# Kernel optimization log

Measured on AMD Instinct MI355X. Metric: run time of the kernel, lower is better.

Reference implementation:

```python
import jax, jax.numpy as jnp
import numpy as np

IN_F = 4096
OUT_F = 4096
RANK = 16
ALPHA = 32
BLOCK = 64  # quantization blocksize along in_features
SCALING = ALPHA / RANK


def setup_inputs() -> dict:
    key = jax.random.key(0)
    k1, k2, k3, k4, k5, k6 = jax.random.split(key, 6)
    x = jax.random.normal(k1, (4, 2048, IN_F), dtype=jnp.float32)
    # int4 codes stored with +8 offset, values in [0, 16)
    q_codes = jax.random.randint(k2, (OUT_F, IN_F), 0, 16, dtype=jnp.int32)
    # per-(row, block) dequant scales
    scales = jax.random.uniform(k3, (OUT_F, IN_F // BLOCK), dtype=jnp.float32) * 0.02
    bias = jax.random.normal(k4, (OUT_F,), dtype=jnp.float32) * 0.02
    lora_A = jax.random.normal(k5, (RANK, IN_F), dtype=jnp.float32) * (1.0 / np.sqrt(IN_F))
    lora_B = jax.random.normal(k6, (OUT_F, RANK), dtype=jnp.float32) * 0.02
    return {"x": x, "q_codes": q_codes, "scales": scales, "bias": bias,
            "lora_A": lora_A, "lora_B": lora_B}


def _dequant(q_codes, scales):
    # [O, I] int4 codes (offset by 8) -> fp32 weight via blockwise scales
    O, I = q_codes.shape
    c = (q_codes.astype(jnp.float32) - 8.0).reshape(O, I // BLOCK, BLOCK)
    return (c * scales[:, :, None]).reshape(O, I)


def reference(x, q_codes, scales, bias, lora_A, lora_B):
    w = _dequant(q_codes, scales)                      # [O, I]
    base = jnp.einsum('bsi,oi->bso', x, w) + bias      # dequant GEMM + bias
    # LoRA branch: dropout(p=0) is identity; x @ (B@A).T == (x @ A.T) @ B.T
    lora = jnp.einsum('bsr,or->bso', jnp.einsum('bsi,ri->bsr', x, lora_A), lora_B)
    return base + lora * SCALING
```

## Files before the change

### kernel.cpp

```cpp
#include <hip/hip_runtime.h>
#include <hip/hip_bf16.h>

#define IN_F   4096
#define OUT_F  4096
#define RANK   16
#define M_TOK  8192
#define SCALING 2.0f

typedef __attribute__((ext_vector_type(8)))  short short8;
typedef __attribute__((ext_vector_type(4)))  float f32x4;
typedef __attribute__((ext_vector_type(16))) float f32x16;
typedef __attribute__((ext_vector_type(4)))  float fvec4;
typedef __attribute__((ext_vector_type(4)))  int   ivec4;
typedef __attribute__((ext_vector_type(4)))  unsigned int uvec4;

__global__ __launch_bounds__(256) void cvt_x(const float* __restrict__ x,
                                             __hip_bfloat16* __restrict__ xb) {
    const size_t nvec = (size_t)M_TOK * IN_F / 8;
    const size_t stride = (size_t)gridDim.x * 256;
    for (size_t idx = (size_t)blockIdx.x * 256 + threadIdx.x; idx < nvec; idx += stride) {
        const size_t i = idx * 8;
        fvec4 a = __builtin_nontemporal_load((const fvec4*)(x + i));
        fvec4 b = __builtin_nontemporal_load((const fvec4*)(x + i + 4));
        union { uvec4 u; __hip_bfloat16 h[8]; } p;
        p.h[0] = __float2bfloat16(a.x);
        p.h[1] = __float2bfloat16(a.y);
        p.h[2] = __float2bfloat16(a.z);
        p.h[3] = __float2bfloat16(a.w);
        p.h[4] = __float2bfloat16(b.x);
        p.h[5] = __float2bfloat16(b.y);
        p.h[6] = __float2bfloat16(b.z);
        p.h[7] = __float2bfloat16(b.w);
        *(uvec4*)(xb + i) = p.u;
    }
}

__global__ __launch_bounds__(256) void dequant_lora(const int* __restrict__ q,
                                                    const float* __restrict__ sc,
                                                    const float* __restrict__ lA,
                                                    const float* __restrict__ lB,
                                                    __hip_bfloat16* __restrict__ W) {
    const int tid = threadIdx.x;
    const int id  = blockIdx.x;
    const int c0  = (id & 3) * 1024 + tid * 4;
    const int o0  = (id >> 2) * 8;

    ivec4 qv[8];
#pragma unroll
    for (int oo = 0; oo < 8; ++oo)
        qv[oo] = __builtin_nontemporal_load(
            (const ivec4*)(q + (size_t)(o0 + oo) * IN_F + c0));

    float sv[8];
#pragma unroll
    for (int oo = 0; oo < 8; ++oo)
        sv[oo] = sc[(o0 + oo) * (IN_F / 64) + (c0 >> 6)];

    fvec4 a[RANK];
#pragma unroll
    for (int r = 0; r < RANK; ++r)
        a[r] = *(const fvec4*)(lA + (size_t)r * IN_F + c0);

#pragma unroll
    for (int oo = 0; oo < 8; ++oo) {
        const float* lbo = lB + (size_t)(o0 + oo) * RANK;
        float l0 = 0.f, l1 = 0.f, l2 = 0.f, l3 = 0.f;
#pragma unroll
        for (int r = 0; r < RANK; ++r) {
            const float br = lbo[r];
            l0 += br * a[r].x; l1 += br * a[r].y;
            l2 += br * a[r].z; l3 += br * a[r].w;
        }
        const float s = sv[oo];
        union { ushort4 u; __hip_bfloat16 h[4]; } p;
        p.h[0] = __float2bfloat16((float)(qv[oo].x - 8) * s + SCALING * l0);
        p.h[1] = __float2bfloat16((float)(qv[oo].y - 8) * s + SCALING * l1);
        p.h[2] = __float2bfloat16((float)(qv[oo].z - 8) * s + SCALING * l2);
        p.h[3] = __float2bfloat16((float)(qv[oo].w - 8) * s + SCALING * l3);
        *(ushort4*)(W + (size_t)(o0 + oo) * IN_F + c0) = p.u;
    }
}


__device__ __forceinline__ void load_lds16(const void* g, void* l) {
    __builtin_amdgcn_global_load_lds(
        (const __attribute__((address_space(1))) unsigned int*)g,
        (__attribute__((address_space(3))) unsigned int*)l, 16, 0, 0);
}

#define MFMA32 __builtin_amdgcn_mfma_f32_32x32x16_bf16

__global__ __launch_bounds__(512, 2) void gemm256_8ph(const __hip_bfloat16* __restrict__ A,
                                                      const __hip_bfloat16* __restrict__ B,
                                                      const float* __restrict__ bias,
                                                      float* __restrict__ C) {
    extern __shared__ __align__(16) char lds[];

    const int tid  = threadIdx.x;
    const int lane = tid & 63;
    const int wave = tid >> 6;

    const int xcd = blockIdx.x & 7;
    const int w64 = blockIdx.x >> 3;
    const int tm  = (xcd >> 1) * 8 + (w64 >> 3);
    const int tn  = (xcd & 1) * 8 + (w64 & 7);

    const __hip_bfloat16* Ab = A + (size_t)tm * 256 * IN_F;
    const __hip_bfloat16* Bb = B + (size_t)tn * 256 * IN_F;

    const int srow = ((lane >> 2) & 15) + ((lane & 1) << 4) + ((wave >> 2) << 5);
    const int skc  = ((((lane >> 1) ^ (lane >> 5)) & 1) << 3) + ((wave & 3) << 4);
    const size_t off0 = (size_t)srow * IN_F + (size_t)skc;

    const __hip_bfloat16* qA0 = Ab + off0;
    const __hip_bfloat16* qA1 = Ab + (size_t)128 * IN_F + off0;
    const __hip_bfloat16* qB0 = Bb + off0;
    const __hip_bfloat16* qB1 = Bb + (size_t)128 * IN_F + off0;

    const int flo32 = (lane & 16)
                    + (((((lane >> 5) ^ (lane >> 3)) & 1)) << 5)
                    + ((lane & 15) << 6);

    const int ah = wave >> 2;
    const int bh = (wave >> 1) & 1;

    const char* aRd[2] = { lds + ah * 16384 + flo32,
                           lds + 65536 + ah * 16384 + flo32 };
    const char* bRd[2] = { lds + 32768 + bh * 16384 + (wave & 1) * 8192 + flo32,
                           lds + 65536 + 32768 + bh * 16384 + (wave & 1) * 8192 + flo32 };

    const int wv1024 = wave * 1024;

#define STAGE2(ps, te, LO) do {                                             \
        const __hip_bfloat16* g_ = (ps) + (te);                             \
        load_lds16(g_,              lds + (LO) + wv1024);                   \
        load_lds16(g_ + 64 * IN_F,  lds + (LO) + 8192 + wv1024);            \
    } while (0)

    STAGE2(qB0, 0,  32768);
    STAGE2(qB1, 0,  49152);
    STAGE2(qA0, 0,  0);
    STAGE2(qA1, 0,  16384);
    STAGE2(qB0, 64, 65536 + 32768);
    STAGE2(qB1, 64, 65536 + 49152);
    asm volatile("s_waitcnt vmcnt(4)" ::: "memory");
    __builtin_amdgcn_s_barrier();

    short8 aF[2][4], bA[4], bB[4];
    f32x16 acc[4][2] = {};

#define TILE(T, CBI) do {                                                          \
        const int t1e = (((T) + 1) & 63) << 6;        \
        const int t2e = (((T) + 2) & 63) << 6;                                     \
                          \
        _Pragma("unroll")                                                          \
        for (int i = 0; i < 2; ++i)                                                \
            _Pragma("unroll")                                                      \
            for (int ks = 0; ks < 4; ++ks)                                         \
                aF[i][ks] = *(const short8*)(aRd[CBI] + i * 4096 + ks * 1024);     \
        _Pragma("unroll")                                                          \
        for (int ks = 0; ks < 4; ++ks)                                             \
            bA[ks] = *(const short8*)(bRd[CBI] + ks * 1024);                       \
        STAGE2(qA0, t1e, ((CBI) ^ 1) * 65536);                                     \
        __builtin_amdgcn_s_setprio(1);                                             \
        _Pragma("unroll")                                                          \
        for (int ks = 0; ks < 4; ++ks) {                                           \
            acc[0][0] = MFMA32(aF[0][ks], bA[ks], acc[0][0], 0, 0, 0);             \
            acc[1][0] = MFMA32(aF[1][ks], bA[ks], acc[1][0], 0, 0, 0);             \
        }                                                                          \
        __builtin_amdgcn_s_setprio(0);                                             \
        __builtin_amdgcn_s_barrier();                     \
                          \
        _Pragma("unroll")                                                          \
        for (int ks = 0; ks < 4; ++ks)                                             \
            bB[ks] = *(const short8*)(bRd[CBI] + 4096 + ks * 1024);                \
        STAGE2(qA1, t1e, ((CBI) ^ 1) * 65536 + 16384);                             \
        __builtin_amdgcn_s_setprio(1);                                             \
        _Pragma("unroll")                                                          \
        for (int ks = 0; ks < 4; ++ks) {                                           \
            acc[0][1] = MFMA32(aF[0][ks], bB[ks], acc[0][1], 0, 0, 0);             \
            acc[1][1] = MFMA32(aF[1][ks], bB[ks], acc[1][1], 0, 0, 0);             \
        }                                                                          \
        __builtin_amdgcn_s_setprio(0);                                             \
        __builtin_amdgcn_s_barrier();                     \
                          \
        _Pragma("unroll")                                                          \
        for (int i = 0; i < 2; ++i)                                                \
            _Pragma("unroll")                                                      \
            for (int ks = 0; ks < 4; ++ks)                                         \
                aF[i][ks] = *(const short8*)(aRd[CBI] + 8192 + i * 4096 + ks * 1024);\
        STAGE2(qB0, t2e, (CBI) * 65536 + 32768);       \
        __builtin_amdgcn_s_setprio(1);                                             \
        _Pragma("unroll")                                                          \
        for (int ks = 0; ks < 4; ++ks) {                                           \
            acc[2][1] = MFMA32(aF[0][ks], bB[ks], acc[2][1], 0, 0, 0);             \
            acc[3][1] = MFMA32(aF[1][ks], bB[ks], acc[3][1], 0, 0, 0);             \
        }                                                                          \
        __builtin_amdgcn_s_setprio(0);                                             \
        __builtin_amdgcn_s_barrier();                \
                          \
        STAGE2(qB1, t2e, (CBI) * 65536 + 49152);       \
        asm volatile("s_waitcnt vmcnt(4)" ::: "memory");      \
        __builtin_amdgcn_s_barrier();                \
        __builtin_amdgcn_s_setprio(1);                                             \
        _Pragma("unroll")                                                          \
        for (int ks = 0; ks < 4; ++ks) {                                           \
            acc[2][0] = MFMA32(aF[0][ks], bA[ks], acc[2][0], 0, 0, 0);             \
            acc[3][0] = MFMA32(aF[1][ks], bA[ks], acc[3][0], 0, 0, 0);             \
        }                                                                          \
        __builtin_amdgcn_s_setprio(0);                                             \
                    \
    } while (0)

    for (int tt = 0; tt < 32; ++tt) {
        TILE(2 * tt,     0);
        TILE(2 * tt + 1, 1);
    }
    asm volatile("s_waitcnt vmcnt(0)" ::: "memory");

    const int cl = lane & 31;
    const int hi = lane >> 5;
    const size_t m_base = (size_t)tm * 256 + (size_t)ah * 128 + hi * 4;
    const int    n_base = tn * 256 + (wave & 3) * 64;
#pragma unroll
    for (int cb = 0; cb < 2; ++cb) {
        const int n = n_base + cb * 32 + cl;
        const float bv = bias[n];
#pragma unroll
        for (int rb = 0; rb < 4; ++rb) {
#pragma unroll
            for (int g = 0; g < 4; ++g) {
                const size_t m0 = m_base + rb * 32 + g * 8;
#pragma unroll
                for (int rr = 0; rr < 4; ++rr)
                    __builtin_nontemporal_store(acc[rb][cb][g * 4 + rr] + bv,
                                                &C[(m0 + rr) * OUT_F + n]);
            }
        }
    }
#undef STAGE2
#undef TILE
}

extern "C" void kernel_launch(void* const* d_in, const int* in_sizes, int n_in,
                              void* d_out, int out_size, void* d_ws, size_t ws_size,
                              hipStream_t stream) {
    const float* x    = (const float*)d_in[0];
    const int*   qc   = (const int*)d_in[1];
    const float* sc   = (const float*)d_in[2];
    const float* bias = (const float*)d_in[3];
    const float* lA   = (const float*)d_in[4];
    const float* lB   = (const float*)d_in[5];
    float* out = (float*)d_out;

    __hip_bfloat16* xb = (__hip_bfloat16*)d_ws;
    __hip_bfloat16* wb = xb + (size_t)M_TOK * IN_F;

    static bool attr_done = false;
    if (!attr_done) {
        (void)hipFuncSetAttribute((const void*)gemm256_8ph,
                                  hipFuncAttributeMaxDynamicSharedMemorySize, 131072);
        attr_done = true;
    }

    cvt_x<<<2048, 256, 0, stream>>>(x, xb);
    dequant_lora<<<2048, 256, 0, stream>>>(qc, sc, lA, lB, wb);
    gemm256_8ph<<<dim3(512), dim3(512), 131072, stream>>>(xb, wb, bias, out);
}
```

Measured before the change: 491.2 us.

## Triple-buffer B tiles in LDS and drop intra-tile barriers

The LDS layout changes from two A/B buffer pairs to two A buffers plus three B buffers, raising dynamic shared memory to 160 KB. The main loop is unrolled with a 6-tile rotation so B buffers cycle on a period of three. This lets three of the four per-tile workgroup barriers be removed, cutting synchronisation stalls between MFMA phases. The cost is more LDS per block and a subtle correctness risk if any write-after-read hazard on the A buffers is no longer covered by a barrier.

Result: no change. 493.8 us (+0.5%).

```diff
diff --git a/kernel.cpp b/kernel.cpp
--- a/kernel.cpp
+++ b/kernel.cpp
@@ -125,9 +125,11 @@
     const int bh = (wave >> 1) & 1;
 
     const char* aRd[2] = { lds + ah * 16384 + flo32,
-                           lds + 65536 + ah * 16384 + flo32 };
-    const char* bRd[2] = { lds + 32768 + bh * 16384 + (wave & 1) * 8192 + flo32,
-                           lds + 65536 + 32768 + bh * 16384 + (wave & 1) * 8192 + flo32 };
+                           lds + 32768 + ah * 16384 + flo32 };
+    const char* bRd[3] = {
+        lds + 65536 +     0 + bh * 16384 + (wave & 1) * 8192 + flo32,
+        lds + 65536 + 32768 + bh * 16384 + (wave & 1) * 8192 + flo32,
+        lds + 65536 + 65536 + bh * 16384 + (wave & 1) * 8192 + flo32 };
 
     const int wv1024 = wave * 1024;
 
@@ -137,19 +139,19 @@
         load_lds16(g_ + 64 * IN_F,  lds + (LO) + 8192 + wv1024);            \
     } while (0)
 
-    STAGE2(qB0, 0,  32768);
-    STAGE2(qB1, 0,  49152);
+    STAGE2(qB0, 0,  65536);
+    STAGE2(qB1, 0,  65536 + 16384);
     STAGE2(qA0, 0,  0);
     STAGE2(qA1, 0,  16384);
     STAGE2(qB0, 64, 65536 + 32768);
-    STAGE2(qB1, 64, 65536 + 49152);
+    STAGE2(qB1, 64, 65536 + 32768 + 16384);
     asm volatile("s_waitcnt vmcnt(4)" ::: "memory");
     __builtin_amdgcn_s_barrier();
 
     short8 aF[2][4], bA[4], bB[4];
     f32x16 acc[4][2] = {};
 
-#define TILE(T, CBI) do {                                                          \
+#define TILE(T, AB, BR, BS) do {                                                   \
         const int t1e = (((T) + 1) & 63) << 6;        \
         const int t2e = (((T) + 2) & 63) << 6;                                     \
                           \
@@ -157,11 +159,11 @@
         for (int i = 0; i < 2; ++i)                                                \
             _Pragma("unroll")                                                      \
             for (int ks = 0; ks < 4; ++ks)                                         \
-                aF[i][ks] = *(const short8*)(aRd[CBI] + i * 4096 + ks * 1024);     \
+                aF[i][ks] = *(const short8*)(aRd[AB] + i * 4096 + ks * 1024);      \
         _Pragma("unroll")                                                          \
         for (int ks = 0; ks < 4; ++ks)                                             \
-            bA[ks] = *(const short8*)(bRd[CBI] + ks * 1024);                       \
-        STAGE2(qA0, t1e, ((CBI) ^ 1) * 65536);                                     \
+            bA[ks] = *(const short8*)(bRd[BR] + ks * 1024);                        \
+        STAGE2(qA0, t1e, ((AB) ^ 1) * 32768);                                      \
         __builtin_amdgcn_s_setprio(1);                                             \
         _Pragma("unroll")                                                          \
         for (int ks = 0; ks < 4; ++ks) {                                           \
@@ -169,12 +171,11 @@
             acc[1][0] = MFMA32(aF[1][ks], bA[ks], acc[1][0], 0, 0, 0);             \
         }                                                                          \
         __builtin_amdgcn_s_setprio(0);                                             \
-        __builtin_amdgcn_s_barrier();                     \
                           \
         _Pragma("unroll")                                                          \
         for (int ks = 0; ks < 4; ++ks)                                             \
-            bB[ks] = *(const short8*)(bRd[CBI] + 4096 + ks * 1024);                \
-        STAGE2(qA1, t1e, ((CBI) ^ 1) * 65536 + 16384);                             \
+            bB[ks] = *(const short8*)(bRd[BR] + 4096 + ks * 1024);                 \
+        STAGE2(qA1, t1e, ((AB) ^ 1) * 32768 + 16384);                              \
         __builtin_amdgcn_s_setprio(1);                                             \
         _Pragma("unroll")                                                          \
         for (int ks = 0; ks < 4; ++ks) {                                           \
@@ -182,14 +183,13 @@
             acc[1][1] = MFMA32(aF[1][ks], bB[ks], acc[1][1], 0, 0, 0);             \
         }                                                                          \
         __builtin_amdgcn_s_setprio(0);                                             \
-        __builtin_amdgcn_s_barrier();                     \
                           \
         _Pragma("unroll")                                                          \
         for (int i = 0; i < 2; ++i)                                                \
             _Pragma("unroll")                                                      \
             for (int ks = 0; ks < 4; ++ks)                                         \
-                aF[i][ks] = *(const short8*)(aRd[CBI] + 8192 + i * 4096 + ks * 1024);\
-        STAGE2(qB0, t2e, (CBI) * 65536 + 32768);       \
+                aF[i][ks] = *(const short8*)(aRd[AB] + 8192 + i * 4096 + ks * 1024);\
+        STAGE2(qB0, t2e, 65536 + (BS) * 32768);                                    \
         __builtin_amdgcn_s_setprio(1);                                             \
         _Pragma("unroll")                                                          \
         for (int ks = 0; ks < 4; ++ks) {                                           \
@@ -197,9 +197,8 @@
             acc[3][1] = MFMA32(aF[1][ks], bB[ks], acc[3][1], 0, 0, 0);             \
         }                                                                          \
         __builtin_amdgcn_s_setprio(0);                                             \
-        __builtin_amdgcn_s_barrier();                \
-                          \
-        STAGE2(qB1, t2e, (CBI) * 65536 + 49152);       \
+                          \
+        STAGE2(qB1, t2e, 65536 + (BS) * 32768 + 16384);                            \
         asm volatile("s_waitcnt vmcnt(4)" ::: "memory");      \
         __builtin_amdgcn_s_barrier();                \
         __builtin_amdgcn_s_setprio(1);                                             \
@@ -209,13 +208,21 @@
             acc[3][0] = MFMA32(aF[1][ks], bA[ks], acc[3][0], 0, 0, 0);             \
         }                                                                          \
         __builtin_amdgcn_s_setprio(0);                                             \
-                    \
     } while (0)
 
-    for (int tt = 0; tt < 32; ++tt) {
-        TILE(2 * tt,     0);
-        TILE(2 * tt + 1, 1);
-    }
+    for (int tt = 0; tt < 10; ++tt) {
+        const int b = tt * 6;
+        TILE(b + 0, 0, 0, 2);
+        TILE(b + 1, 1, 1, 0);
+        TILE(b + 2, 0, 2, 1);
+        TILE(b + 3, 1, 0, 2);
+        TILE(b + 4, 0, 1, 0);
+        TILE(b + 5, 1, 2, 1);
+    }
+    TILE(60, 0, 0, 2);
+    TILE(61, 1, 1, 0);
+    TILE(62, 0, 2, 1);
+    TILE(63, 1, 0, 2);
     asm volatile("s_waitcnt vmcnt(0)" ::: "memory");
 
     const int cl = lane & 31;
@@ -259,11 +266,11 @@
     static bool attr_done = false;
     if (!attr_done) {
         (void)hipFuncSetAttribute((const void*)gemm256_8ph,
-                                  hipFuncAttributeMaxDynamicSharedMemorySize, 131072);
+                                  hipFuncAttributeMaxDynamicSharedMemorySize, 163840);
         attr_done = true;
     }
 
     cvt_x<<<2048, 256, 0, stream>>>(x, xb);
     dequant_lora<<<2048, 256, 0, stream>>>(qc, sc, lA, lB, wb);
-    gemm256_8ph<<<dim3(512), dim3(512), 131072, stream>>>(xb, wb, bias, out);
-}
+    gemm256_8ph<<<dim3(512), dim3(512), 163840, stream>>>(xb, wb, bias, out);
+}
```
